# Performance work log

Measured on AMD Instinct MI355X. Metric: run time of the kernel, lower is better.

The kernel has to match this reference:

```python
import jax, jax.numpy as jnp
import numpy as np

# Dims: B INRs, N probe points, d_in=2 coords, hidden H, out D_OUT, proj P
B, N, D_IN, H, D_OUT, P = 128, 4096, 2, 128, 3, 128
W0_SIREN = 30.0  # SIREN frequency scale
LN_EPS = 1e-5


def setup_inputs() -> dict:
    key = jax.random.key(0)
    ks = jax.random.split(key, 12)
    sn = lambda k, shape, sc: (jax.random.normal(k, shape, dtype=jnp.float32) * sc)
    return {
        # per-sample SIREN params, torch layout: weight [b, in, out, 1], bias [b, out, 1]
        "w0": sn(ks[0], (B, D_IN, H, 1), 1.0 / D_IN),
        "w1": sn(ks[1], (B, H, H, 1), np.sqrt(6.0 / H) / W0_SIREN),
        "w2": sn(ks[2], (B, H, D_OUT, 1), np.sqrt(6.0 / H) / W0_SIREN),
        "b0": sn(ks[3], (B, H, 1), 0.1),
        "b1": sn(ks[4], (B, H, 1), 0.1),
        "b2": sn(ks[5], (B, D_OUT, 1), 0.1),
        # learned probe coordinates, initialized U[-1, 1) as in the module
        "inputs": jax.random.uniform(ks[6], (1, N, D_IN), dtype=jnp.float32, minval=-1.0, maxval=1.0),
        # projection (num_inputs -> proj_dim) + LayerNorm params, one per probed layer (4 total)
        "pw": sn(ks[7], (4, N, P), 1.0 / np.sqrt(N)),
        "pb": jnp.zeros((4, P), jnp.float32),
        "ln_g": jnp.ones((4, P), jnp.float32),
        "ln_b": jnp.zeros((4, P), jnp.float32),
    }


def _layernorm(x, g, b):
    m = jnp.mean(x, axis=-1, keepdims=True)
    v = jnp.mean(jnp.square(x - m), axis=-1, keepdims=True)
    return (x - m) * jax.lax.rsqrt(v + LN_EPS) * g + b


def reference(w0, w1, w2, b0, b1, b2, inputs, pw, pb, ln_g, ln_b):
    b = w0.shape[0]
    x = jnp.broadcast_to(inputs, (b,) + inputs.shape[1:])  # [b, n, d_in]

    def lin(h, W, bb):
        # per-sample linear: [b,n,i] @ [b,i,o] + [b,1,o]
        return jnp.einsum('bni,bio->bno', h, W[..., 0]) + bb[:, None, :, 0]

    h1 = jnp.sin(W0_SIREN * lin(x, w0, b0))   # [b, n, H]
    h2 = jnp.sin(W0_SIREN * lin(h1, w1, b1))  # [b, n, H]
    h3 = lin(h2, w2, b2)                      # [b, n, D_OUT] (last layer: no sine)
    feats = [x, h1, h2, h3]  # probe features per node layer (input coords + activations)

    outs = []
    for i, f in enumerate(feats):
        # permute to [b, dim_i, n], project n -> P, then LayerNorm over P
        z = jnp.einsum('bnd,np->bdp', f, pw[i]) + pb[i]
        outs.append(_layernorm(z, ln_g[i], ln_b[i]))
    return jnp.concatenate(outs, axis=1)  # [b, d_in + H + H + D_OUT, P]
```

## Files before the change

kernel.cpp:

```cpp
#include <hip/hip_runtime.h>


typedef unsigned short u16;
typedef __attribute__((ext_vector_type(8))) short short8;
typedef __attribute__((ext_vector_type(4))) short short4v;
typedef __attribute__((ext_vector_type(4))) float f32x4;
typedef __attribute__((ext_vector_type(4))) float float4v;

#define DEV __device__ __forceinline__
#define R30 4.774648292756860f

DEV float b2f(u16 h){ return __uint_as_float(((unsigned)h) << 16); }
DEV u16 f2b(float f){
  unsigned u = __float_as_uint(f);
  return (u16)((u + 0x7FFFu + ((u >> 16) & 1u)) >> 16);
}
DEV unsigned pkcvt(float a, float b){
#if __has_builtin(__builtin_amdgcn_cvt_pk_bf16_f32)
  typedef __attribute__((ext_vector_type(2))) __bf16 bf16x2;
  bf16x2 v = __builtin_amdgcn_cvt_pk_bf16_f32(a, b);
  return *(unsigned*)&v;
#else
  return (unsigned)f2b(a) | (((unsigned)f2b(b)) << 16);
#endif
}
DEV short8 pack8(const float* f){
  union { unsigned u[4]; short8 s; } r;
#pragma unroll
  for (int j = 0; j < 4; j++) r.u[j] = pkcvt(f[2*j], f[2*j+1]);
  return r.s;
}
DEV float sin_rev(float r){
  r = r - rintf(r);
#if __has_builtin(__builtin_amdgcn_sinf)
  return __builtin_amdgcn_sinf(r);
#else
  return __sinf(r * 6.283185307179586f);
#endif
}
template<int C> DEV float dpp_add(float x){
  int yi = __builtin_amdgcn_update_dpp(0, __float_as_int(x), C, 0xF, 0xF, true);
  return x + __int_as_float(yi);
}
DEV float sum16(float x){
  x = dpp_add<0x128>(x); x = dpp_add<0x124>(x);
  x = dpp_add<0x122>(x); x = dpp_add<0x121>(x);
  return x;
}

DEV int is_bf16_fmt(const void* lng){ return *(const unsigned*)lng == 0x3F803F80u; }
struct In {
  const float* f; const u16* h; int bf;
  DEV In(const void* p, int b_) : f((const float*)p), h((const u16*)p), bf(b_) {}
  DEV float at(size_t i) const { return bf ? b2f(h[i]) : f[i]; }
};

__global__ __launch_bounds__(256) void k_prep(const void* pwv, const void* inpv,
                                              const void* lngv,
                                              u16* __restrict__ pwT,
                                              float* __restrict__ xbuf){
  const int bf = is_bf16_fmt(lngv);
  const int t = threadIdx.x;
  if (blockIdx.x == 256){
    In inp(inpv, bf);
    for (int i = t; i < 8192; i += 256) xbuf[i] = inp.at(i);
    return;
  }
  In pw(pwv, bf);
  __shared__ u16 tile[64 * 129];
  const int layer = blockIdx.x >> 6;
  const int n0 = (blockIdx.x & 63) * 64;
  const size_t base = ((size_t)layer * 4096 + n0) * 128;
#pragma unroll
  for (int k = 0; k < 32; k++){
    int idx = k * 256 + t, n = idx >> 7, p = idx & 127;
    tile[n * 129 + p] = f2b(pw.at(base + (size_t)n * 128 + p));
  }
  __syncthreads();
  u16* dst = pwT + (size_t)layer * 128 * 4096 + n0;
#pragma unroll
  for (int k = 0; k < 32; k++){
    int idx = k * 256 + t, p = idx >> 6, n = idx & 63;
    dst[(size_t)p * 4096 + n] = tile[n * 129 + p];
  }
}

#define S_NK 136
#define S_T  40

template<bool PARTIAL>
__global__ __launch_bounds__(512, 2)
void k_main(const void* w0v, const void* w1v, const void* w2v,
            const void* b0v, const void* b1v, const void* b2v,
            const void* pbv, const void* lgv, const void* lbv,
            const u16* __restrict__ pwTg, const float* __restrict__ xbuf,
            float* __restrict__ outp, int TS){
  __shared__ __align__(16) u16 sh1nk[2][32 * S_NK];
  __shared__ __align__(16) u16 sh1T[2][128 * S_T];
  __shared__ __align__(16) u16 sh2T[2][128 * S_T];
  __shared__ __align__(16) u16 sxT[2][16 * S_T];
  __shared__ float sW2[512];
  __shared__ float sb2[4];
  __shared__ float sPB[512], sG[512], sBB[512];

  float* sP1 = (float*)&sh1nk[0][0];
  float* sP2 = (float*)&sh1T[0][0];
  float* sM  = (float*)&sh2T[0][0];
  float* sI  = (float*)&sh2T[0][0] + 512;

  const int bf = is_bf16_fmt(lgv);
  In w0(w0v, bf), w1(w1v, bf), w2(w2v, bf), b0(b0v, bf), b1(b1v, bf),
     b2(b2v, bf), pb(pbv, bf), lg(lgv, bf), lb(lbv, bf);

  const int t = threadIdx.x;
  const int b = blockIdx.x & 127, sseg = blockIdx.x >> 7;
  const int lane = t & 63, wave = t >> 6, quad = lane >> 4, r16 = lane & 15;
  const int oo = wave * 16 + r16;

  if (t >= 256 && t < 384){
    int i = t - 256;
    sW2[i * 4 + 0] = w2.at(((size_t)b * 128 + i) * 3 + 0);
    sW2[i * 4 + 1] = w2.at(((size_t)b * 128 + i) * 3 + 1);
    sW2[i * 4 + 2] = w2.at(((size_t)b * 128 + i) * 3 + 2);
    sW2[i * 4 + 3] = 0.f;
  }
  if (t < 4) sb2[t] = (t < 3) ? b2.at(b * 3 + t) : 0.f;
  sPB[t] = pb.at(t); sG[t] = lg.at(t); sBB[t] = lb.at(t);
  for (int k = t; k < 2 * 16 * S_T; k += 512) sxT[0][k] = 0;

  const int p1n = t >> 4, p1hb = (t & 15) * 8;
  float w00[8], w01[8], b00[8];
#pragma unroll
  for (int j = 0; j < 8; j++){
    w00[j] = w0.at((size_t)b * 256 + p1hb + j) * R30;
    w01[j] = w0.at((size_t)b * 256 + 128 + p1hb + j) * R30;
    b00[j] = b0.at((size_t)b * 128 + p1hb + j) * R30;
  }
  const int p2h = t & 127, p2nb = (t >> 7) * 8;
  const float q00 = w0.at((size_t)b * 256 + p2h) * R30;
  const float q01 = w0.at((size_t)b * 256 + 128 + p2h) * R30;
  const float qb0 = b0.at((size_t)b * 128 + p2h) * R30;
  const float bias1r = b1.at((size_t)b * 128 + oo) * R30;

  short8 w1f[4];
#pragma unroll
  for (int ks = 0; ks < 4; ks++){
#pragma unroll
    for (int j = 0; j < 8; j++)
      w1f[ks][j] = (short)f2b(w1.at((size_t)b * 16384 +
                                    (size_t)(ks * 32 + quad * 8 + j) * 128 + oo));
  }
  short8 a1s = {0,0,0,0,0,0,0,0};
  if (r16 == 0){
#pragma unroll
    for (int j = 0; j < 8; j++) a1s[j] = (short)0x3F80;
  }

  const u16* pwbase = pwTg + (size_t)oo * 4096 + quad * 8;

  const f32x4 zz = {0.f,0.f,0.f,0.f};
  f32x4 az1[8], az2[8], ay[8], az0 = zz, az3 = zz;
#pragma unroll
  for (int i = 0; i < 8; i++){ az1[i] = zz; az2[i] = zz; ay[i] = zz; }

  short8 pwf[4];
#pragma unroll
  for (int L = 0; L < 4; L++)
    pwf[L] = *(const short8*)(pwbase + (size_t)L * 524288 + sseg * TS * 32);

  __syncthreads();

  for (int nt = 0; nt < TS; nt++){
    const int buf = nt & 1;
    const int n0 = (sseg * TS + nt) * 32;

    if (t < 64){
      int n = t >> 1, c = t & 1;
      sxT[buf][c * S_T + n] = f2b(xbuf[(size_t)(n0 + n) * 2 + c]);
    }
    {
      float2 xv = *(const float2*)(xbuf + (size_t)(n0 + p1n) * 2);
      float vv[8];
#pragma unroll
      for (int j = 0; j < 8; j++)
        vv[j] = sin_rev(fmaf(xv.y, w01[j], fmaf(xv.x, w00[j], b00[j])));
      *(short8*)&sh1nk[buf][p1n * S_NK + p1hb] = pack8(vv);
    }
    {
      float4v xq[4];
#pragma unroll
      for (int q = 0; q < 4; q++)
        xq[q] = *(const float4v*)(xbuf + (size_t)(n0 + p2nb) * 2 + q * 4);
      float vv[8];
#pragma unroll
      for (int j = 0; j < 8; j++){
        float x0 = xq[j >> 1][(j & 1) * 2], x1 = xq[j >> 1][(j & 1) * 2 + 1];
        vv[j] = sin_rev(fmaf(x1, q01, fmaf(x0, q00, qb0)));
      }
      *(short8*)&sh1T[buf][p2h * S_T + p2nb] = pack8(vv);
    }
    __syncthreads();

    short8 pwn[4];
    {
      const int nn = (nt + 1 < TS) ? nt + 1 : nt;
      const int n0n = (sseg * TS + nn) * 32;
#pragma unroll
      for (int L = 0; L < 4; L++)
        pwn[L] = *(const short8*)(pwbase + (size_t)L * 524288 + n0n);
    }

    f32x4 h0 = zz, h1a = zz;
#pragma unroll
    for (int ks = 0; ks < 4; ks++){
      h0  = __builtin_amdgcn_mfma_f32_16x16x32_bf16(
              *(short8*)&sh1nk[buf][r16 * S_NK + ks * 32 + quad * 8], w1f[ks], h0, 0, 0, 0);
      h1a = __builtin_amdgcn_mfma_f32_16x16x32_bf16(
              *(short8*)&sh1nk[buf][(16 + r16) * S_NK + ks * 32 + quad * 8], w1f[ks], h1a, 0, 0, 0);
    }
    az0 = __builtin_amdgcn_mfma_f32_16x16x32_bf16(
            *(short8*)&sxT[buf][r16 * S_T + quad * 8], pwf[0], az0, 0, 0, 0);
#pragma unroll
    for (int mb = 0; mb < 8; mb++)
      az1[mb] = __builtin_amdgcn_mfma_f32_16x16x32_bf16(
                  *(short8*)&sh1T[buf][(mb * 16 + r16) * S_T + quad * 8],
                  pwf[1], az1[mb], 0, 0, 0);
    az3 = __builtin_amdgcn_mfma_f32_16x16x32_bf16(a1s, pwf[3], az3, 0, 0, 0);
    {
      unsigned* d0 = (unsigned*)&sh2T[buf][oo * S_T + quad * 4];
      d0[0] = pkcvt(sin_rev(fmaf(h0[0], R30, bias1r)),
                    sin_rev(fmaf(h0[1], R30, bias1r)));
      d0[1] = pkcvt(sin_rev(fmaf(h0[2], R30, bias1r)),
                    sin_rev(fmaf(h0[3], R30, bias1r)));
      unsigned* d1 = (unsigned*)&sh2T[buf][oo * S_T + 16 + quad * 4];
      d1[0] = pkcvt(sin_rev(fmaf(h1a[0], R30, bias1r)),
                    sin_rev(fmaf(h1a[1], R30, bias1r)));
      d1[1] = pkcvt(sin_rev(fmaf(h1a[2], R30, bias1r)),
                    sin_rev(fmaf(h1a[3], R30, bias1r)));
    }
    __syncthreads();

#pragma unroll
    for (int mb = 0; mb < 8; mb++){
      short8 a = *(short8*)&sh2T[buf][(mb * 16 + r16) * S_T + quad * 8];
      az2[mb] = __builtin_amdgcn_mfma_f32_16x16x32_bf16(a, pwf[2], az2[mb], 0, 0, 0);
      ay[mb]  = __builtin_amdgcn_mfma_f32_16x16x32_bf16(a, pwf[3], ay[mb], 0, 0, 0);
    }

#pragma unroll
    for (int L = 0; L < 4; L++) pwf[L] = pwn[L];
  }

  const int p = oo;
  float S3 = (quad == 0) ? az3[0] : 0.f;
  S3 += __shfl_xor(S3, 16, 64); S3 += __shfl_xor(S3, 32, 64);
  float z3v[3];
#pragma unroll
  for (int d = 0; d < 3; d++){
    float a = 0.f;
#pragma unroll
    for (int mb = 0; mb < 8; mb++)
#pragma unroll
      for (int r = 0; r < 4; r++)
        a = fmaf(sW2[(mb * 16 + quad * 4 + r) * 4 + d], ay[mb][r], a);
    a += __shfl_xor(a, 16, 64); a += __shfl_xor(a, 32, 64);
    z3v[d] = a + sb2[d] * S3;
  }

  if (PARTIAL){
    float* zp = outp + ((size_t)(sseg * 128 + b)) * 261 * 128;
    if (quad == 0){
#pragma unroll
      for (int r = 0; r < 2; r++) zp[(size_t)r * 128 + p] = az0[r];
#pragma unroll
      for (int d = 0; d < 3; d++) zp[(size_t)(258 + d) * 128 + p] = z3v[d];
    }
#pragma unroll
    for (int mb = 0; mb < 8; mb++)
#pragma unroll
      for (int r = 0; r < 4; r++){
        int drow = mb * 16 + quad * 4 + r;
        zp[(size_t)(2 + drow) * 128 + p]   = az1[mb][r];
        zp[(size_t)(130 + drow) * 128 + p] = az2[mb][r];
      }
    return;
  }

  __syncthreads();
  const float pb0v = sPB[p],       pb1v = sPB[128 + p];
  const float pb2v = sPB[256 + p], pb3v = sPB[384 + p];

  auto rowsum = [&](float v, int row, bool wr){
    float s1 = sum16(v), s2 = sum16(v * v);
    if (wr && r16 == 0){ sP1[row * 8 + wave] = s1; sP2[row * 8 + wave] = s2; }
  };
#pragma unroll
  for (int r = 0; r < 2; r++) rowsum(az0[r] + pb0v, r, quad == 0);
#pragma unroll
  for (int mb = 0; mb < 8; mb++)
#pragma unroll
    for (int r = 0; r < 4; r++)
      rowsum(az1[mb][r] + pb1v, 2 + mb * 16 + quad * 4 + r, true);
#pragma unroll
  for (int mb = 0; mb < 8; mb++)
#pragma unroll
    for (int r = 0; r < 4; r++)
      rowsum(az2[mb][r] + pb2v, 130 + mb * 16 + quad * 4 + r, true);
#pragma unroll
  for (int d = 0; d < 3; d++) rowsum(z3v[d] + pb3v, 258 + d, quad == 0);
  __syncthreads();

  if (t < 261){
    float s1 = 0.f, s2 = 0.f;
#pragma unroll
    for (int w = 0; w < 8; w++){ s1 += sP1[t * 8 + w]; s2 += sP2[t * 8 + w]; }
    float m = s1 * (1.f / 128.f);
    float var = fmaf(-m, m, s2 * (1.f / 128.f));
    sM[t] = m;
    sI[t] = rsqrtf(fmaxf(var, 0.f) + 1e-5f);
  }
  __syncthreads();

  const size_t ob = (size_t)b * 261 * 128;
  auto emit = [&](float v, int row, int grp){
    outp[ob + (size_t)row * 128 + p] =
      (v - sM[row]) * sI[row] * sG[grp * 128 + p] + sBB[grp * 128 + p];
  };
  if (quad == 0){
#pragma unroll
    for (int r = 0; r < 2; r++) emit(az0[r] + pb0v, r, 0);
#pragma unroll
    for (int d = 0; d < 3; d++) emit(z3v[d] + pb3v, 258 + d, 3);
  }
#pragma unroll
  for (int mb = 0; mb < 8; mb++)
#pragma unroll
    for (int r = 0; r < 4; r++)
      emit(az1[mb][r] + pb1v, 2 + mb * 16 + quad * 4 + r, 1);
#pragma unroll
  for (int mb = 0; mb < 8; mb++)
#pragma unroll
    for (int r = 0; r < 4; r++)
      emit(az2[mb][r] + pb2v, 130 + mb * 16 + quad * 4 + r, 2);
}

__global__ __launch_bounds__(256)
void k_ln(const float* __restrict__ zp, const void* pbv, const void* lgv,
          const void* lbv, float* __restrict__ out, int split){
  const int bf = is_bf16_fmt(lgv);
  In pb(pbv, bf), lg(lgv, bf), lb(lbv, bf);
  const int lane = threadIdx.x & 63;
  const int row = blockIdx.x * 4 + (threadIdx.x >> 6);
  const int b = row / 261, d = row % 261;
  const int grp = (d < 2) ? 0 : (d < 130) ? 1 : (d < 258) ? 2 : 3;
  const int p0 = lane * 2;
  float v0 = pb.at(grp * 128 + p0), v1 = pb.at(grp * 128 + p0 + 1);
  for (int s2 = 0; s2 < split; s2++){
    const float* zr = zp + ((size_t)(s2 * 128 + b) * 261 + d) * 128;
    v0 += zr[p0]; v1 += zr[p0 + 1];
  }
  float s1 = v0 + v1, s2s = v0 * v0 + v1 * v1;
#pragma unroll
  for (int o = 1; o < 64; o <<= 1){
    s1 += __shfl_xor(s1, o, 64);
    s2s += __shfl_xor(s2s, o, 64);
  }
  float m = s1 * (1.f / 128.f);
  float var = fmaf(-m, m, s2s * (1.f / 128.f));
  float inv = rsqrtf(fmaxf(var, 0.f) + 1e-5f);
  float2 o2;
  o2.x = (v0 - m) * inv * lg.at(grp * 128 + p0)     + lb.at(grp * 128 + p0);
  o2.y = (v1 - m) * inv * lg.at(grp * 128 + p0 + 1) + lb.at(grp * 128 + p0 + 1);
  *(float2*)(out + (size_t)row * 128 + p0) = o2;
}

extern "C" void kernel_launch(void* const* d_in, const int* in_sizes, int n_in,
                              void* d_out, int out_size, void* d_ws, size_t ws_size,
                              hipStream_t stream){
  const void* w0  = d_in[0];
  const void* w1  = d_in[1];
  const void* w2  = d_in[2];
  const void* b0  = d_in[3];
  const void* b1  = d_in[4];
  const void* b2  = d_in[5];
  const void* inp = d_in[6];
  const void* pw  = d_in[7];
  const void* pb  = d_in[8];
  const void* lng = d_in[9];
  const void* lnb = d_in[10];
  float* out = (float*)d_out;

  u16* pwT    = (u16*)d_ws;
  float* xbuf = (float*)((char*)d_ws + (size_t)4 * 128 * 4096 * 2);
  const size_t zoff = (size_t)4 * 128 * 4096 * 2 + 8192 * 4;
  float* zp = (float*)((char*)d_ws + zoff);
  const size_t seg = (size_t)128 * 261 * 128 * 4;

  const int split = (ws_size >= zoff + 2 * seg) ? 2 : 1;

  k_prep<<<257, 256, 0, stream>>>(pw, inp, lng, pwT, xbuf);
  if (split == 2){
    k_main<true><<<256, 512, 0, stream>>>(w0, w1, w2, b0, b1, b2,
        pb, lng, lnb, pwT, xbuf, zp, 64);
    k_ln<<<(128 * 261) / 4, 256, 0, stream>>>(zp, pb, lng, lnb, out, 2);
  } else {
    k_main<false><<<128, 512, 0, stream>>>(w0, w1, w2, b0, b1, b2,
        pb, lng, lnb, pwT, xbuf, out, 128);
  }
}
```

Measured before the change: 261.0 us.

## Software-pipeline layer-1 sine tile generation into the previous iteration

Moves the computation of the next tile's first-layer sine activations and coordinate tile into the current iteration, writing into the alternate double buffer before the mid-iteration barrier. This removes one __syncthreads per tile and lets the x loads and sine math overlap with the MFMA work. A prologue fills buffer 0 before the loop. Register pressure rises because the x values for the next tile are held across the MFMA section.

```diff
diff --git a/kernel.cpp b/kernel.cpp
--- a/kernel.cpp
+++ b/kernel.cpp
@@ -163,52 +163,59 @@
 #pragma unroll
   for (int i = 0; i < 8; i++){ az1[i] = zz; az2[i] = zz; ay[i] = zz; }
 
+  auto do_W = [&](int wbuf, float2 xv1, const float4v* xqv){
+    if ((t & 15) == 0){
+      sxT[wbuf][p1n] = f2b(xv1.x);
+      sxT[wbuf][S_T + p1n] = f2b(xv1.y);
+    }
+    {
+      float vv[8];
+#pragma unroll
+      for (int j = 0; j < 8; j++)
+        vv[j] = sin_rev(fmaf(xv1.y, w01[j], fmaf(xv1.x, w00[j], b00[j])));
+      *(short8*)&sh1nk[wbuf][p1n * S_NK + p1hb] = pack8(vv);
+    }
+    {
+      float vv[8];
+#pragma unroll
+      for (int j = 0; j < 8; j++){
+        float x0 = xqv[j >> 1][(j & 1) * 2], x1 = xqv[j >> 1][(j & 1) * 2 + 1];
+        vv[j] = sin_rev(fmaf(x1, q01, fmaf(x0, q00, qb0)));
+      }
+      *(short8*)&sh1T[wbuf][p2h * S_T + p2nb] = pack8(vv);
+    }
+  };
+
+  const int n0first = sseg * TS * 32;
   short8 pwf[4];
 #pragma unroll
   for (int L = 0; L < 4; L++)
-    pwf[L] = *(const short8*)(pwbase + (size_t)L * 524288 + sseg * TS * 32);
-
+    pwf[L] = *(const short8*)(pwbase + (size_t)L * 524288 + n0first);
+  {
+    float2 xv1 = *(const float2*)(xbuf + (size_t)(n0first + p1n) * 2);
+    float4v xqv[4];
+#pragma unroll
+    for (int q = 0; q < 4; q++)
+      xqv[q] = *(const float4v*)(xbuf + (size_t)(n0first + p2nb) * 2 + q * 4);
+    __syncthreads();
+    do_W(0, xv1, xqv);
+  }
   __syncthreads();
 
   for (int nt = 0; nt < TS; nt++){
     const int buf = nt & 1;
-    const int n0 = (sseg * TS + nt) * 32;
-
-    if (t < 64){
-      int n = t >> 1, c = t & 1;
-      sxT[buf][c * S_T + n] = f2b(xbuf[(size_t)(n0 + n) * 2 + c]);
-    }
-    {
-      float2 xv = *(const float2*)(xbuf + (size_t)(n0 + p1n) * 2);
-      float vv[8];
-#pragma unroll
-      for (int j = 0; j < 8; j++)
-        vv[j] = sin_rev(fmaf(xv.y, w01[j], fmaf(xv.x, w00[j], b00[j])));
-      *(short8*)&sh1nk[buf][p1n * S_NK + p1hb] = pack8(vv);
-    }
-    {
-      float4v xq[4];
-#pragma unroll
-      for (int q = 0; q < 4; q++)
-        xq[q] = *(const float4v*)(xbuf + (size_t)(n0 + p2nb) * 2 + q * 4);
-      float vv[8];
-#pragma unroll
-      for (int j = 0; j < 8; j++){
-        float x0 = xq[j >> 1][(j & 1) * 2], x1 = xq[j >> 1][(j & 1) * 2 + 1];
-        vv[j] = sin_rev(fmaf(x1, q01, fmaf(x0, q00, qb0)));
-      }
-      *(short8*)&sh1T[buf][p2h * S_T + p2nb] = pack8(vv);
-    }
-    __syncthreads();
+    const int nn = (nt + 1 < TS) ? nt + 1 : nt;
+    const int n0n = (sseg * TS + nn) * 32;
 
     short8 pwn[4];
-    {
-      const int nn = (nt + 1 < TS) ? nt + 1 : nt;
-      const int n0n = (sseg * TS + nn) * 32;
-#pragma unroll
-      for (int L = 0; L < 4; L++)
-        pwn[L] = *(const short8*)(pwbase + (size_t)L * 524288 + n0n);
-    }
+#pragma unroll
+    for (int L = 0; L < 4; L++)
+      pwn[L] = *(const short8*)(pwbase + (size_t)L * 524288 + n0n);
+    float2 xv1 = *(const float2*)(xbuf + (size_t)(n0n + p1n) * 2);
+    float4v xqv[4];
+#pragma unroll
+    for (int q = 0; q < 4; q++)
+      xqv[q] = *(const float4v*)(xbuf + (size_t)(n0n + p2nb) * 2 + q * 4);
 
     f32x4 h0 = zz, h1a = zz;
 #pragma unroll
@@ -238,6 +245,8 @@
       d1[1] = pkcvt(sin_rev(fmaf(h1a[2], R30, bias1r)),
                     sin_rev(fmaf(h1a[3], R30, bias1r)));
     }
+
+    do_W(buf ^ 1, xv1, xqv);
     __syncthreads();
 
 #pragma unroll
```

Result: no change. 265.7 us (+1.8%).
